# Kernel optimization log

Hardware: AMD Instinct MI355X
Metric: run time of the kernel (lower is better)

Reference implementation:

```python
import jax, jax.numpy as jnp
import numpy as np

B, S, E, H = 2, 2048, 1024, 16
D = E // H  # d_k = n_wires = 64


def setup_inputs() -> dict:
    key = jax.random.key(0)
    ks = jax.random.split(key, 6)
    x = jax.random.normal(ks[0], (B, S, E), dtype=jnp.float32)
    scale = 0.02
    Wq = jax.random.normal(ks[1], (E, E), dtype=jnp.float32) * scale
    Wk = jax.random.normal(ks[2], (E, E), dtype=jnp.float32) * scale
    Wv = jax.random.normal(ks[3], (E, E), dtype=jnp.float32) * scale
    Wc = jax.random.normal(ks[4], (E, E), dtype=jnp.float32) * scale
    bc = jnp.zeros((E,), dtype=jnp.float32)
    return {"x": x, "Wq": Wq, "Wk": Wk, "Wv": Wv, "Wc": Wc, "bc": bc}


def _split_heads(t):
    # [B,S,E] -> [B,H,S,D]
    return t.reshape(B, S, H, D).transpose(0, 2, 1, 3)


def _quantum(t):
    # RX(theta_i) per wire + CNOT ladder + per-wire PauliZ expectation:
    # <Z_j> = prod_{i<=j} cos(theta_i)  (closed form of the circuit)
    return jnp.cumprod(jnp.cos(t), axis=-1)


def reference(x, Wq, Wk, Wv, Wc, bc):
    q = _quantum(_split_heads(x @ Wq.T))  # [B,H,S,D]
    k = _quantum(_split_heads(x @ Wk.T))
    v = _quantum(_split_heads(x @ Wv.T))
    scores = jnp.einsum('bhsd,bhtd->bhst', q, k) / jnp.sqrt(jnp.float32(D))
    attn = jax.nn.softmax(scores, axis=-1)
    out = jnp.einsum('bhst,bhtd->bhsd', attn, v)  # [B,H,S,D]
    out = out.transpose(0, 2, 1, 3).reshape(B, S, E)
    return out @ Wc.T + bc
```

## Files before the change

kernel.cpp:

```cpp
#include <hip/hip_runtime.h>
#include <hip/hip_bf16.h>

constexpr int Bc = 2, Sc = 2048, Ec = 1024, Hc = 16, Dc = 64;
constexpr int Mrows = Bc * Sc;
constexpr int Kdim  = Ec;

typedef float  floatx4 __attribute__((ext_vector_type(4)));
typedef short  shortx8 __attribute__((ext_vector_type(8)));

__device__ inline unsigned short f2bf(float f) {
    union { __hip_bfloat16 h; unsigned short u; } cv;
    cv.h = __float2bfloat16(f);
    return cv.u;
}
__device__ inline float bf2f(unsigned short u) {
    union { unsigned int i; float f; } c; c.i = ((unsigned int)u) << 16; return c.f;
}
__device__ inline float exp2_fast(float x) {
#if __has_builtin(__builtin_amdgcn_exp2f)
    return __builtin_amdgcn_exp2f(x);
#else
    return __expf(x * 0.69314718056f);
#endif
}

__device__ __forceinline__ void gll16(const void* g, void* lds) {
    __builtin_amdgcn_global_load_lds(
        (const __attribute__((address_space(1))) void*)g,
        (__attribute__((address_space(3))) void*)lds, 16, 0, 0);
}

__global__ __launch_bounds__(256) void convert_all_kernel(
    const float* __restrict__ x,  const float* __restrict__ Wq,
    const float* __restrict__ Wk, const float* __restrict__ Wv,
    const float* __restrict__ Wc,
    unsigned short* __restrict__ xb,  unsigned short* __restrict__ Wqb,
    unsigned short* __restrict__ Wkb, unsigned short* __restrict__ Wvb,
    unsigned short* __restrict__ Wcb)
{
    const long t = (long)blockIdx.x * 256 + threadIdx.x;
    const long i = t * 4;
    const float* src; unsigned short* dst; long off;
    if (i < 4194304) { src = x; dst = xb; off = i; }
    else {
        long j = i - 4194304;
        int wsel = (int)(j >> 20);
        off = j & 1048575;
        src = (wsel == 0) ? Wq : (wsel == 1) ? Wk : (wsel == 2) ? Wv : Wc;
        dst = (wsel == 0) ? Wqb : (wsel == 1) ? Wkb : (wsel == 2) ? Wvb : Wcb;
    }
    float4 v = *(const float4*)(src + off);
    unsigned short tmp[4] __attribute__((aligned(8)));
    tmp[0] = f2bf(v.x); tmp[1] = f2bf(v.y); tmp[2] = f2bf(v.z); tmp[3] = f2bf(v.w);
    *(uint2*)(dst + off) = *(uint2*)tmp;
}

__global__ __launch_bounds__(256) void proj_mfma_kernel(
    const unsigned short* __restrict__ Ab,
    const unsigned short* __restrict__ Wqb,
    const unsigned short* __restrict__ Wkb,
    const unsigned short* __restrict__ Wvb,
    unsigned short* __restrict__ oq,
    unsigned short* __restrict__ ok,
    unsigned short* __restrict__ ov)
{
    __shared__ __align__(16) char smem[33792];
    float (*Cs)[132] = (float(*)[132])smem;
    __shared__ float Sp[64][9];

    const int z = blockIdx.z;
    const unsigned short* Wb = (z == 0) ? Wqb : (z == 1) ? Wkb : Wvb;
    unsigned short* out      = (z == 0) ? oq  : (z == 1) ? ok  : ov;
    const int mode = (z == 2) ? 1 : 0;

    const int tid = threadIdx.x;
    const int lane = tid & 63;
    const int w = tid >> 6, l15 = tid & 15, quad = (tid >> 4) & 3;
    const int wq = w >> 1, wn = w & 1;
    const int m0 = blockIdx.x * 128;
    const int n0 = blockIdx.y * 128;
    const int h0 = n0 >> 6;
    const int sw = l15 & 7;

    floatx4 acc[4][4];
    #pragma unroll
    for (int ms = 0; ms < 4; ++ms)
        #pragma unroll
        for (int ns = 0; ns < 4; ++ns)
            #pragma unroll
            for (int e = 0; e < 4; ++e) acc[ms][ns][e] = 0.0f;

    for (int k0 = 0; k0 < Kdim; k0 += 64) {
        #pragma unroll
        for (int j = 0; j < 4; ++j) {
            int idx = j * 64 + lane;
            int row = 32 * w + (idx >> 3);
            int cg  = ((idx & 7) ^ (idx >> 3)) & 7;
            gll16(Ab + (size_t)(m0 + row) * Kdim + k0 + cg * 8,
                  smem + 4096 * w + 1024 * j);
            gll16(Wb + (size_t)(n0 + row) * Kdim + k0 + cg * 8,
                  smem + 16384 + 4096 * w + 1024 * j);
        }
        __syncthreads();
        #pragma unroll
        for (int ks = 0; ks < 2; ++ks) {
            shortx8 af[4], bf[4];
            #pragma unroll
            for (int ms = 0; ms < 4; ++ms)
                af[ms] = *(shortx8*)(smem + (64 * wq + 16 * ms + l15) * 128
                                     + (((4 * ks + quad) ^ sw) << 4));
            #pragma unroll
            for (int ns = 0; ns < 4; ++ns)
                bf[ns] = *(shortx8*)(smem + 16384 + (64 * wn + 16 * ns + l15) * 128
                                     + (((4 * ks + quad) ^ sw) << 4));
            #pragma unroll
            for (int ms = 0; ms < 4; ++ms)
                #pragma unroll
                for (int ns = 0; ns < 4; ++ns)
                    acc[ms][ns] = __builtin_amdgcn_mfma_f32_16x16x32_bf16(
                        af[ms], bf[ns], acc[ms][ns], 0, 0, 0);
        }
        __syncthreads();
    }

    const int b = m0 >> 11;
    const int sbase = m0 & (Sc - 1);

    for (int pass = 0; pass < 2; ++pass) {
        if (wq == pass) {
            #pragma unroll
            for (int ms = 0; ms < 4; ++ms)
                #pragma unroll
                for (int ns = 0; ns < 4; ++ns)
                    #pragma unroll
                    for (int r = 0; r < 4; ++r)
                        Cs[16 * ms + 4 * quad + r][64 * wn + 16 * ns + l15] =
                            __cosf(acc[ms][ns][r]);
        }
        __syncthreads();
        #pragma unroll
        for (int t = tid; t < 512; t += 256) {
            int row = t >> 3, seg = t & 7;
            float pr = 1.0f;
            #pragma unroll
            for (int c = 0; c < 16; ++c) pr *= Cs[row][seg * 16 + c];
            Sp[row][seg] = pr;
        }
        __syncthreads();
        if (mode == 0) {
            #pragma unroll
            for (int t = tid; t < 512; t += 256) {
                int row = t >> 3, seg = t & 7;
                float p = 1.0f;
                for (int j = (seg & 4); j < seg; ++j) p *= Sp[row][j];
                unsigned short tmp[16] __attribute__((aligned(16)));
                #pragma unroll
                for (int c = 0; c < 16; ++c) { p *= Cs[row][seg * 16 + c]; tmp[c] = f2bf(p); }
                int h = h0 + (seg >> 2);
                int s = sbase + pass * 64 + row;
                size_t base = (((size_t)b * Hc + h) * Sc + s) * Dc + (seg & 3) * 16;
                *(shortx8*)(out + base)     = *(shortx8*)&tmp[0];
                *(shortx8*)(out + base + 8) = *(shortx8*)&tmp[8];
            }
            __syncthreads();
        } else {
            #pragma unroll
            for (int t = tid; t < 512; t += 256) {
                int row = t >> 3, seg = t & 7;
                float p = 1.0f;
                for (int j = (seg & 4); j < seg; ++j) p *= Sp[row][j];
                #pragma unroll
                for (int c = 0; c < 16; ++c) { p *= Cs[row][seg * 16 + c]; Cs[row][seg * 16 + c] = p; }
            }
            __syncthreads();
            #pragma unroll
            for (int t = tid; t < 512; t += 256) {
                int col = t >> 2, chunk = t & 3;
                int h = h0 + (col >> 6), d = col & 63;
                unsigned short tmp[16] __attribute__((aligned(16)));
                #pragma unroll
                for (int j = 0; j < 16; ++j) tmp[j] = f2bf(Cs[chunk * 16 + j][col]);
                size_t base = (((size_t)b * Hc + h) * Dc + d) * Sc
                              + sbase + pass * 64 + chunk * 16;
                *(shortx8*)(out + base)     = *(shortx8*)&tmp[0];
                *(shortx8*)(out + base + 8) = *(shortx8*)&tmp[8];
            }
            __syncthreads();
        }
    }
}

__global__ __launch_bounds__(256) void attn_mfma_kernel(
    const unsigned short* __restrict__ qg,
    const unsigned short* __restrict__ kg,
    const unsigned short* __restrict__ vtg,
    unsigned short* __restrict__ o1,
    unsigned short* __restrict__ o2,
    float* __restrict__ lpart)
{
    __shared__ __align__(16) char smem[34816];
    unsigned short (*Pq)[72] = (unsigned short(*)[72])(smem + 16384);

    const int tid  = threadIdx.x;
    const int lane = tid & 63;
    const int w    = tid >> 6;
    const int l15  = tid & 15;
    const int quad = (tid >> 4) & 3;
    const int qb   = blockIdx.x;
    const int half = blockIdx.y;
    const int bh   = blockIdx.z;
    const int sw   = l15 & 7;

    const unsigned short* qp = qg  + (size_t)bh * Sc * Dc;
    const unsigned short* kp = kg  + (size_t)bh * Sc * Dc;
    const unsigned short* vp = vtg + (size_t)bh * Dc * Sc;

    int qrow[2];
    shortx8 qf[2][2];
    #pragma unroll
    for (int qs = 0; qs < 2; ++qs) {
        qrow[qs] = qb * 128 + 32 * w + 16 * qs + l15;
        qf[qs][0] = *(const shortx8*)(qp + (size_t)qrow[qs] * Dc + 8 * quad);
        qf[qs][1] = *(const shortx8*)(qp + (size_t)qrow[qs] * Dc + 32 + 8 * quad);
    }

    floatx4 Oacc[2][4];
    #pragma unroll
    for (int qs = 0; qs < 2; ++qs)
        #pragma unroll
        for (int mt = 0; mt < 4; ++mt)
            #pragma unroll
            for (int e = 0; e < 4; ++e) Oacc[qs][mt][e] = 0.0f;
    float lsum[2] = {0.0f, 0.0f};

    const float cexp = 0.125f * 1.442695041f;

    for (int kt = half * 16; kt < half * 16 + 16; ++kt) {
        #pragma unroll
        for (int j = 0; j < 2; ++j) {
            int idx = j * 64 + lane;
            int row = 16 * w + (idx >> 3);
            int cg  = ((idx & 7) ^ (idx >> 3)) & 7;
            gll16(kp + (size_t)(kt * 64 + row) * Dc + cg * 8,
                  smem + 2048 * w + 1024 * j);
            gll16(vp + (size_t)row * Sc + kt * 64 + cg * 8,
                  smem + 8192 + 2048 * w + 1024 * j);
        }
        __syncthreads();

        shortx8 kf[2][4], vf[2][4];
        #pragma unroll
        for (int ks = 0; ks < 2; ++ks)
            #pragma unroll
            for (int mt = 0; mt < 4; ++mt) {
                int off = (16 * mt + l15) * 128 + (((4 * ks + quad) ^ sw) << 4);
                kf[ks][mt] = *(shortx8*)(smem + off);
                vf[ks][mt] = *(shortx8*)(smem + 8192 + off);
            }

        #pragma unroll
        for (int qs = 0; qs < 2; ++qs) {
            floatx4 st[4];
            #pragma unroll
            for (int mt = 0; mt < 4; ++mt)
                #pragma unroll
                for (int e = 0; e < 4; ++e) st[mt][e] = 0.0f;
            #pragma unroll
            for (int ks = 0; ks < 2; ++ks)
                #pragma unroll
                for (int mt = 0; mt < 4; ++mt)
                    st[mt] = __builtin_amdgcn_mfma_f32_16x16x32_bf16(
                        kf[ks][mt], qf[qs][ks], st[mt], 0, 0, 0);

            float rs = 0.0f;
            #pragma unroll
            for (int mt = 0; mt < 4; ++mt) {
                float p0 = exp2_fast(st[mt][0] * cexp);
                float p1 = exp2_fast(st[mt][1] * cexp);
                float p2 = exp2_fast(st[mt][2] * cexp);
                float p3 = exp2_fast(st[mt][3] * cexp);
                rs += (p0 + p1) + (p2 + p3);
                unsigned short tmp[4] __attribute__((aligned(8)));
                tmp[0] = f2bf(p0); tmp[1] = f2bf(p1); tmp[2] = f2bf(p2); tmp[3] = f2bf(p3);
                *(uint2*)&Pq[32 * w + 16 * qs + l15][16 * mt + 4 * quad] = *(uint2*)tmp;
            }
            lsum[qs] += rs;

            #pragma unroll
            for (int ks = 0; ks < 2; ++ks) {
                shortx8 pf = *(shortx8*)&Pq[32 * w + 16 * qs + l15][32 * ks + 8 * quad];
                #pragma unroll
                for (int mt = 0; mt < 4; ++mt)
                    Oacc[qs][mt] = __builtin_amdgcn_mfma_f32_16x16x32_bf16(
                        vf[ks][mt], pf, Oacc[qs][mt], 0, 0, 0);
            }
        }
        __syncthreads();
    }

    const int b = bh >> 4, hh = bh & 15;
    unsigned short* opart = half ? o2 : o1;
    float* lp = lpart + ((size_t)half * (Bc * Hc) + bh) * Sc;
    #pragma unroll
    for (int qs = 0; qs < 2; ++qs) {
        float l = lsum[qs];
        l += __shfl_xor(l, 16, 64);
        l += __shfl_xor(l, 32, 64);
        if (quad == 0) lp[qrow[qs]] = l;
        #pragma unroll
        for (int mt = 0; mt < 4; ++mt) {
            unsigned short tmp[4] __attribute__((aligned(8)));
            #pragma unroll
            for (int r = 0; r < 4; ++r) tmp[r] = f2bf(Oacc[qs][mt][r]);
            size_t base = ((size_t)b * Sc + qrow[qs]) * Ec + hh * 64 + 16 * mt + 4 * quad;
            *(uint2*)(opart + base) = *(uint2*)tmp;
        }
    }
}

__global__ __launch_bounds__(256) void combine_kernel(
    unsigned short* __restrict__ o1,
    const unsigned short* __restrict__ o2,
    const float* __restrict__ lpart)
{
    const size_t t = (size_t)blockIdx.x * 256 + threadIdx.x;
    const size_t base = t * 8;
    const int e = (int)(base & (Ec - 1));
    const int h = e >> 6;
    const size_t bs = base >> 10;
    const int b = (int)(bs >> 11), s = (int)(bs & (Sc - 1));
    const int bh = b * Hc + h;
    const float l = lpart[(size_t)bh * Sc + s]
                  + lpart[(size_t)(Bc * Hc + bh) * Sc + s];
    const float inv = 1.0f / l;
    uint4 a = *(const uint4*)(o1 + base);
    uint4 c = *(const uint4*)(o2 + base);
    const unsigned short* ua = (const unsigned short*)&a;
    const unsigned short* uc = (const unsigned short*)&c;
    unsigned short r[8] __attribute__((aligned(16)));
    #pragma unroll
    for (int i = 0; i < 8; ++i)
        r[i] = f2bf((bf2f(ua[i]) + bf2f(uc[i])) * inv);
    *(uint4*)(o1 + base) = *(uint4*)r;
}

__global__ __launch_bounds__(256) void outproj_mfma_kernel(
    const unsigned short* __restrict__ Ab,
    const unsigned short* __restrict__ Wb,
    const float* __restrict__ bias,
    float* __restrict__ out)
{
    __shared__ __align__(16) char smem[24576];

    const int tid = threadIdx.x;
    const int lane = tid & 63;
    const int w = tid >> 6, l15 = tid & 15, quad = (tid >> 4) & 3;
    const int wq = w >> 1, wn = w & 1;
    const int m0 = blockIdx.x * 64;
    const int n0 = blockIdx.y * 128;
    const int sw = l15 & 7;

    floatx4 acc[2][4];
    #pragma unroll
    for (int ms = 0; ms < 2; ++ms)
        #pragma unroll
        for (int ns = 0; ns < 4; ++ns)
            #pragma unroll
            for (int e = 0; e < 4; ++e) acc[ms][ns][e] = 0.0f;

    for (int k0 = 0; k0 < Kdim; k0 += 64) {
        #pragma unroll
        for (int j = 0; j < 2; ++j) {
            int idx = j * 64 + lane;
            int row = 16 * w + (idx >> 3);
            int cg  = ((idx & 7) ^ (idx >> 3)) & 7;
            gll16(Ab + (size_t)(m0 + row) * Kdim + k0 + cg * 8,
                  smem + 2048 * w + 1024 * j);
        }
        #pragma unroll
        for (int j = 0; j < 4; ++j) {
            int idx = j * 64 + lane;
            int row = 32 * w + (idx >> 3);
            int cg  = ((idx & 7) ^ (idx >> 3)) & 7;
            gll16(Wb + (size_t)(n0 + row) * Kdim + k0 + cg * 8,
                  smem + 8192 + 4096 * w + 1024 * j);
        }
        __syncthreads();
        #pragma unroll
        for (int ks = 0; ks < 2; ++ks) {
            shortx8 af[2], bf[4];
            #pragma unroll
            for (int ms = 0; ms < 2; ++ms)
                af[ms] = *(shortx8*)(smem + (32 * wq + 16 * ms + l15) * 128
                                     + (((4 * ks + quad) ^ sw) << 4));
            #pragma unroll
            for (int ns = 0; ns < 4; ++ns)
                bf[ns] = *(shortx8*)(smem + 8192 + (64 * wn + 16 * ns + l15) * 128
                                     + (((4 * ks + quad) ^ sw) << 4));
            #pragma unroll
            for (int ms = 0; ms < 2; ++ms)
                #pragma unroll
                for (int ns = 0; ns < 4; ++ns)
                    acc[ms][ns] = __builtin_amdgcn_mfma_f32_16x16x32_bf16(
                        af[ms], bf[ns], acc[ms][ns], 0, 0, 0);
        }
        __syncthreads();
    }

    #pragma unroll
    for (int ns = 0; ns < 4; ++ns) {
        const float bv = bias[n0 + 64 * wn + 16 * ns + l15];
        #pragma unroll
        for (int ms = 0; ms < 2; ++ms)
            #pragma unroll
            for (int r = 0; r < 4; ++r) {
                int m = m0 + 32 * wq + 16 * ms + 4 * quad + r;
                out[(size_t)m * Kdim + n0 + 64 * wn + 16 * ns + l15] = acc[ms][ns][r] + bv;
            }
    }
}

extern "C" void kernel_launch(void* const* d_in, const int* in_sizes, int n_in,
                              void* d_out, int out_size, void* d_ws, size_t ws_size,
                              hipStream_t stream) {
    const float* x  = (const float*)d_in[0];
    const float* Wq = (const float*)d_in[1];
    const float* Wk = (const float*)d_in[2];
    const float* Wv = (const float*)d_in[3];
    const float* Wc = (const float*)d_in[4];
    const float* bc = (const float*)d_in[5];
    float* out = (float*)d_out;

    char* p = (char*)d_ws;
    unsigned short* xb   = (unsigned short*)(p);
    unsigned short* Wqb  = (unsigned short*)(p + (8u << 20));
    unsigned short* Wkb  = (unsigned short*)(p + (10u << 20));
    unsigned short* Wvb  = (unsigned short*)(p + (12u << 20));
    unsigned short* Wcb  = (unsigned short*)(p + (14u << 20));
    unsigned short* qb_  = (unsigned short*)(p + (16u << 20));
    unsigned short* kb_  = (unsigned short*)(p + (24u << 20));
    unsigned short* vtb  = (unsigned short*)(p + (32u << 20));
    unsigned short* attb = (unsigned short*)(p + (40u << 20));
    unsigned short* o2b  = xb;
    float*          lpart = (float*)(p + (8u << 20));

    hipLaunchKernelGGL(convert_all_kernel, dim3(8192), dim3(256), 0, stream,
                       x, Wq, Wk, Wv, Wc, xb, Wqb, Wkb, Wvb, Wcb);

    hipLaunchKernelGGL(proj_mfma_kernel, dim3(Mrows / 128, Ec / 128, 3), dim3(256), 0, stream,
                       xb, Wqb, Wkb, Wvb, qb_, kb_, vtb);

    hipLaunchKernelGGL(attn_mfma_kernel, dim3(Sc / 128, 2, Bc * Hc), dim3(256), 0, stream,
                       qb_, kb_, vtb, attb, o2b, lpart);

    hipLaunchKernelGGL(combine_kernel, dim3(Mrows * Ec / (256 * 8)), dim3(256), 0, stream,
                       attb, o2b, lpart);

    hipLaunchKernelGGL(outproj_mfma_kernel, dim3(Mrows / 64, Ec / 128), dim3(256), 0, stream,
                       attb, Wcb, bc, out);
}
```

Measured before the change: 212.8 us.

## Double-buffer K/V tiles, fold softmax scale into Q, use cheaper bf16 packing

The attention loop moves from 64-key tiles with two barriers per tile to 32-key tiles held in double-buffered LDS, so the next tile's global-to-LDS load is issued while the current one is computed. The softmax scale and log2(e) factor are folded into Q when the projection stores it, which removes one multiply per score. Every bf16 conversion is replaced by a hand-written round-half-up pack of two floats into one dword. In exchange the loop runs twice as many iterations with smaller MFMA batches, and the rounding differs slightly from round-to-nearest-even with no NaN handling. The new P-tile indexing (Pq[16*w+l15]) and per-wave loads should be checked against the 128-query block layout, because rows appear to be shared between the qs iterations.

```diff
diff --git a/kernel.cpp b/kernel.cpp
--- a/kernel.cpp
+++ b/kernel.cpp
@@ -5,13 +5,15 @@
 constexpr int Mrows = Bc * Sc;
 constexpr int Kdim  = Ec;
 
+#define QSCALE 0.18033688011112042f
+
 typedef float  floatx4 __attribute__((ext_vector_type(4)));
 typedef short  shortx8 __attribute__((ext_vector_type(8)));
 
-__device__ inline unsigned short f2bf(float f) {
-    union { __hip_bfloat16 h; unsigned short u; } cv;
-    cv.h = __float2bfloat16(f);
-    return cv.u;
+__device__ __forceinline__ unsigned int pack2bf(float a, float b) {
+    union { float f; unsigned int u; } ca, cb;
+    ca.f = a; cb.f = b;
+    return ((ca.u + 0x8000u) >> 16) | ((cb.u + 0x8000u) & 0xffff0000u);
 }
 __device__ inline float bf2f(unsigned short u) {
     union { unsigned int i; float f; } c; c.i = ((unsigned int)u) << 16; return c.f;
@@ -50,9 +52,10 @@
         dst = (wsel == 0) ? Wqb : (wsel == 1) ? Wkb : (wsel == 2) ? Wvb : Wcb;
     }
     float4 v = *(const float4*)(src + off);
-    unsigned short tmp[4] __attribute__((aligned(8)));
-    tmp[0] = f2bf(v.x); tmp[1] = f2bf(v.y); tmp[2] = f2bf(v.z); tmp[3] = f2bf(v.w);
-    *(uint2*)(dst + off) = *(uint2*)tmp;
+    uint2 u;
+    u.x = pack2bf(v.x, v.y);
+    u.y = pack2bf(v.z, v.w);
+    *(uint2*)(dst + off) = u;
 }
 
 __global__ __launch_bounds__(256) void proj_mfma_kernel(
@@ -72,6 +75,7 @@
     const unsigned short* Wb = (z == 0) ? Wqb : (z == 1) ? Wkb : Wvb;
     unsigned short* out      = (z == 0) ? oq  : (z == 1) ? ok  : ov;
     const int mode = (z == 2) ? 1 : 0;
+    const float osc = (z == 0) ? QSCALE : 1.0f;
 
     const int tid = threadIdx.x;
     const int lane = tid & 63;
@@ -153,14 +157,18 @@
                 int row = t >> 3, seg = t & 7;
                 float p = 1.0f;
                 for (int j = (seg & 4); j < seg; ++j) p *= Sp[row][j];
-                unsigned short tmp[16] __attribute__((aligned(16)));
-                #pragma unroll
-                for (int c = 0; c < 16; ++c) { p *= Cs[row][seg * 16 + c]; tmp[c] = f2bf(p); }
+                unsigned int dw[8];
+                #pragma unroll
+                for (int c2 = 0; c2 < 8; ++c2) {
+                    p *= Cs[row][seg * 16 + 2 * c2];     float a = p * osc;
+                    p *= Cs[row][seg * 16 + 2 * c2 + 1]; float bb = p * osc;
+                    dw[c2] = pack2bf(a, bb);
+                }
                 int h = h0 + (seg >> 2);
                 int s = sbase + pass * 64 + row;
                 size_t base = (((size_t)b * Hc + h) * Sc + s) * Dc + (seg & 3) * 16;
-                *(shortx8*)(out + base)     = *(shortx8*)&tmp[0];
-                *(shortx8*)(out + base + 8) = *(shortx8*)&tmp[8];
+                *(uint4*)(out + base)     = *(uint4*)&dw[0];
+                *(uint4*)(out + base + 8) = *(uint4*)&dw[4];
             }
             __syncthreads();
         } else {
@@ -177,13 +185,15 @@
             for (int t = tid; t < 512; t += 256) {
                 int col = t >> 2, chunk = t & 3;
                 int h = h0 + (col >> 6), d = col & 63;
-                unsigned short tmp[16] __attribute__((aligned(16)));
-                #pragma unroll
-                for (int j = 0; j < 16; ++j) tmp[j] = f2bf(Cs[chunk * 16 + j][col]);
+                unsigned int dw[8];
+                #pragma unroll
+                for (int j2 = 0; j2 < 8; ++j2)
+                    dw[j2] = pack2bf(Cs[chunk * 16 + 2 * j2][col],
+                                     Cs[chunk * 16 + 2 * j2 + 1][col]);
                 size_t base = (((size_t)b * Hc + h) * Dc + d) * Sc
                               + sbase + pass * 64 + chunk * 16;
-                *(shortx8*)(out + base)     = *(shortx8*)&tmp[0];
-                *(shortx8*)(out + base + 8) = *(shortx8*)&tmp[8];
+                *(uint4*)(out + base)     = *(uint4*)&dw[0];
+                *(uint4*)(out + base + 8) = *(uint4*)&dw[4];
             }
             __syncthreads();
         }
@@ -198,8 +208,9 @@
     unsigned short* __restrict__ o2,
     float* __restrict__ lpart)
 {
-    __shared__ __align__(16) char smem[34816];
-    unsigned short (*Pq)[72] = (unsigned short(*)[72])(smem + 16384);
+    __shared__ __align__(16) unsigned short Ks[2][32][64];
+    __shared__ __align__(16) unsigned short VTs[2][64][32];
+    __shared__ __align__(16) unsigned short Pq[64][72];
 
     const int tid  = threadIdx.x;
     const int lane = tid & 63;
@@ -233,69 +244,70 @@
             for (int e = 0; e < 4; ++e) Oacc[qs][mt][e] = 0.0f;
     float lsum[2] = {0.0f, 0.0f};
 
-    const float cexp = 0.125f * 1.442695041f;
-
-    for (int kt = half * 16; kt < half * 16 + 16; ++kt) {
-        #pragma unroll
-        for (int j = 0; j < 2; ++j) {
-            int idx = j * 64 + lane;
-            int row = 16 * w + (idx >> 3);
-            int cg  = ((idx & 7) ^ (idx >> 3)) & 7;
-            gll16(kp + (size_t)(kt * 64 + row) * Dc + cg * 8,
-                  smem + 2048 * w + 1024 * j);
-            gll16(vp + (size_t)row * Sc + kt * 64 + cg * 8,
-                  smem + 8192 + 2048 * w + 1024 * j);
-        }
-        __syncthreads();
-
-        shortx8 kf[2][4], vf[2][4];
+    const unsigned short* kgl = kp
+        + (size_t)(half * 1024 + 8 * w + (lane >> 3)) * Dc
+        + (((lane & 7) ^ ((lane >> 3) & 7)) * 8);
+    const unsigned short* vgl = vp
+        + (size_t)(16 * w + (lane >> 2)) * Sc + half * 1024 + (lane & 3) * 8;
+
+    gll16(kgl, &Ks[0][8 * w][0]);
+    gll16(vgl, &VTs[0][16 * w][0]);
+
+    for (int it = 0; it < 32; ++it) {
+        const int buf = it & 1;
+        __syncthreads();
+        if (it + 1 < 32) {
+            const int nb = (it + 1) & 1;
+            gll16(kgl + (size_t)(it + 1) * 32 * Dc, &Ks[nb][8 * w][0]);
+            gll16(vgl + (it + 1) * 32,              &VTs[nb][16 * w][0]);
+        }
+
+        shortx8 kf[2][2], vf[4];
         #pragma unroll
         for (int ks = 0; ks < 2; ++ks)
             #pragma unroll
-            for (int mt = 0; mt < 4; ++mt) {
-                int off = (16 * mt + l15) * 128 + (((4 * ks + quad) ^ sw) << 4);
-                kf[ks][mt] = *(shortx8*)(smem + off);
-                vf[ks][mt] = *(shortx8*)(smem + 8192 + off);
-            }
+            for (int mtp = 0; mtp < 2; ++mtp)
+                kf[ks][mtp] = *(shortx8*)&Ks[buf][16 * mtp + l15]
+                                            [(((4 * ks + quad) ^ sw) & 7) * 8];
+        #pragma unroll
+        for (int mt = 0; mt < 4; ++mt)
+            vf[mt] = *(shortx8*)&VTs[buf][16 * mt + l15][8 * quad];
 
         #pragma unroll
         for (int qs = 0; qs < 2; ++qs) {
-            floatx4 st[4];
-            #pragma unroll
-            for (int mt = 0; mt < 4; ++mt)
-                #pragma unroll
-                for (int e = 0; e < 4; ++e) st[mt][e] = 0.0f;
+            floatx4 st[2];
+            #pragma unroll
+            for (int mtp = 0; mtp < 2; ++mtp)
+                #pragma unroll
+                for (int e = 0; e < 4; ++e) st[mtp][e] = 0.0f;
             #pragma unroll
             for (int ks = 0; ks < 2; ++ks)
                 #pragma unroll
-                for (int mt = 0; mt < 4; ++mt)
-                    st[mt] = __builtin_amdgcn_mfma_f32_16x16x32_bf16(
-                        kf[ks][mt], qf[qs][ks], st[mt], 0, 0, 0);
+                for (int mtp = 0; mtp < 2; ++mtp)
+                    st[mtp] = __builtin_amdgcn_mfma_f32_16x16x32_bf16(
+                        kf[ks][mtp], qf[qs][ks], st[mtp], 0, 0, 0);
 
             float rs = 0.0f;
             #pragma unroll
-            for (int mt = 0; mt < 4; ++mt) {
-                float p0 = exp2_fast(st[mt][0] * cexp);
-                float p1 = exp2_fast(st[mt][1] * cexp);
-                float p2 = exp2_fast(st[mt][2] * cexp);
-                float p3 = exp2_fast(st[mt][3] * cexp);
+            for (int mtp = 0; mtp < 2; ++mtp) {
+                float p0 = exp2_fast(st[mtp][0]);
+                float p1 = exp2_fast(st[mtp][1]);
+                float p2 = exp2_fast(st[mtp][2]);
+                float p3 = exp2_fast(st[mtp][3]);
                 rs += (p0 + p1) + (p2 + p3);
-                unsigned short tmp[4] __attribute__((aligned(8)));
-                tmp[0] = f2bf(p0); tmp[1] = f2bf(p1); tmp[2] = f2bf(p2); tmp[3] = f2bf(p3);
-                *(uint2*)&Pq[32 * w + 16 * qs + l15][16 * mt + 4 * quad] = *(uint2*)tmp;
+                uint2 u;
+                u.x = pack2bf(p0, p1);
+                u.y = pack2bf(p2, p3);
+                *(uint2*)&Pq[16 * w + l15][16 * mtp + 4 * quad] = u;
             }
             lsum[qs] += rs;
 
-            #pragma unroll
-            for (int ks = 0; ks < 2; ++ks) {
-                shortx8 pf = *(shortx8*)&Pq[32 * w + 16 * qs + l15][32 * ks + 8 * quad];
-                #pragma unroll
-                for (int mt = 0; mt < 4; ++mt)
-                    Oacc[qs][mt] = __builtin_amdgcn_mfma_f32_16x16x32_bf16(
-                        vf[ks][mt], pf, Oacc[qs][mt], 0, 0, 0);
-            }
-        }
-        __syncthreads();
+            shortx8 pf = *(shortx8*)&Pq[16 * w + l15][8 * quad];
+            #pragma unroll
+            for (int mt = 0; mt < 4; ++mt)
+                Oacc[qs][mt] = __builtin_amdgcn_mfma_f32_16x16x32_bf16(
+                    vf[mt], pf, Oacc[qs][mt], 0, 0, 0);
+        }
     }
 
     const int b = bh >> 4, hh = bh & 15;
@@ -309,11 +321,11 @@
         if (quad == 0) lp[qrow[qs]] = l;
         #pragma unroll
         for (int mt = 0; mt < 4; ++mt) {
-            unsigned short tmp[4] __attribute__((aligned(8)));
-            #pragma unroll
-            for (int r = 0; r < 4; ++r) tmp[r] = f2bf(Oacc[qs][mt][r]);
+            uint2 u;
+            u.x = pack2bf(Oacc[qs][mt][0], Oacc[qs][mt][1]);
+            u.y = pack2bf(Oacc[qs][mt][2], Oacc[qs][mt][3]);
             size_t base = ((size_t)b * Sc + qrow[qs]) * Ec + hh * 64 + 16 * mt + 4 * quad;
-            *(uint2*)(opart + base) = *(uint2*)tmp;
+            *(uint2*)(opart + base) = u;
         }
     }
 }
@@ -337,11 +349,12 @@
     uint4 c = *(const uint4*)(o2 + base);
     const unsigned short* ua = (const unsigned short*)&a;
     const unsigned short* uc = (const unsigned short*)&c;
-    unsigned short r[8] __attribute__((aligned(16)));
-    #pragma unroll
-    for (int i = 0; i < 8; ++i)
-        r[i] = f2bf((bf2f(ua[i]) + bf2f(uc[i])) * inv);
-    *(uint4*)(o1 + base) = *(uint4*)r;
+    unsigned int dw[4];
+    #pragma unroll
+    for (int i = 0; i < 4; ++i)
+        dw[i] = pack2bf((bf2f(ua[2 * i]) + bf2f(uc[2 * i])) * inv,
+                        (bf2f(ua[2 * i + 1]) + bf2f(uc[2 * i + 1])) * inv);
+    *(uint4*)(o1 + base) = *(uint4*)dw;
 }
 
 __global__ __launch_bounds__(256) void outproj_mfma_kernel(
```

After: 214.2 us. About the same (+0.7%).

## Fuse pipeline into one cooperative persistent kernel with grid syncs

Applied to the files above, without the earlier changes.

Replaces the five separate launches with a single cooperative kernel of 512 blocks that runs convert, QKV projection, attention and output projection as phases separated by grid.sync. Attention no longer splits keys into two halves, so the combine kernel goes away. The softmax scale is folded into Q at projection time, bf16 packing uses a manual round-to-nearest, and the projection tile shrinks to 64x128. The aim is to remove launch gaps and the combine pass, at the cost of fewer blocks (512) and less parallelism in attention, plus grid-wide barriers.

```diff
diff --git a/kernel.cpp b/kernel.cpp
--- a/kernel.cpp
+++ b/kernel.cpp
@@ -1,20 +1,22 @@
 #include <hip/hip_runtime.h>
 #include <hip/hip_bf16.h>
+#include <hip/hip_cooperative_groups.h>
+
+namespace cg = cooperative_groups;
 
 constexpr int Bc = 2, Sc = 2048, Ec = 1024, Hc = 16, Dc = 64;
 constexpr int Mrows = Bc * Sc;
 constexpr int Kdim  = Ec;
 
+#define QSCALE 0.18033688011112042f
+
 typedef float  floatx4 __attribute__((ext_vector_type(4)));
 typedef short  shortx8 __attribute__((ext_vector_type(8)));
 
-__device__ inline unsigned short f2bf(float f) {
-    union { __hip_bfloat16 h; unsigned short u; } cv;
-    cv.h = __float2bfloat16(f);
-    return cv.u;
-}
-__device__ inline float bf2f(unsigned short u) {
-    union { unsigned int i; float f; } c; c.i = ((unsigned int)u) << 16; return c.f;
+__device__ __forceinline__ unsigned int pack2bf(float a, float b) {
+    union { float f; unsigned int u; } ca, cb;
+    ca.f = a; cb.f = b;
+    return ((ca.u + 0x8000u) >> 16) | ((cb.u + 0x8000u) & 0xffff0000u);
 }
 __device__ inline float exp2_fast(float x) {
 #if __has_builtin(__builtin_amdgcn_exp2f)
@@ -30,7 +32,9 @@
         (__attribute__((address_space(3))) void*)lds, 16, 0, 0);
 }
 
-__global__ __launch_bounds__(256) void convert_all_kernel(
+
+__device__ __forceinline__ void phase_convert(
+    int bx, int tid,
     const float* __restrict__ x,  const float* __restrict__ Wq,
     const float* __restrict__ Wk, const float* __restrict__ Wv,
     const float* __restrict__ Wc,
@@ -38,135 +42,145 @@
     unsigned short* __restrict__ Wkb, unsigned short* __restrict__ Wvb,
     unsigned short* __restrict__ Wcb)
 {
-    const long t = (long)blockIdx.x * 256 + threadIdx.x;
-    const long i = t * 4;
-    const float* src; unsigned short* dst; long off;
-    if (i < 4194304) { src = x; dst = xb; off = i; }
-    else {
-        long j = i - 4194304;
-        int wsel = (int)(j >> 20);
-        off = j & 1048575;
-        src = (wsel == 0) ? Wq : (wsel == 1) ? Wk : (wsel == 2) ? Wv : Wc;
-        dst = (wsel == 0) ? Wqb : (wsel == 1) ? Wkb : (wsel == 2) ? Wvb : Wcb;
-    }
-    float4 v = *(const float4*)(src + off);
-    unsigned short tmp[4] __attribute__((aligned(8)));
-    tmp[0] = f2bf(v.x); tmp[1] = f2bf(v.y); tmp[2] = f2bf(v.z); tmp[3] = f2bf(v.w);
-    *(uint2*)(dst + off) = *(uint2*)tmp;
-}
-
-__global__ __launch_bounds__(256) void proj_mfma_kernel(
-    const unsigned short* __restrict__ Ab,
+    const long gtid = (long)bx * 256 + tid;
+    for (long t = gtid; t < 2097152; t += 131072) {
+        const long i = t * 4;
+        const float* src; unsigned short* dst; long off;
+        if (i < 4194304) { src = x; dst = xb; off = i; }
+        else {
+            long j = i - 4194304;
+            int wsel = (int)(j >> 20);
+            off = j & 1048575;
+            src = (wsel == 0) ? Wq : (wsel == 1) ? Wk : (wsel == 2) ? Wv : Wc;
+            dst = (wsel == 0) ? Wqb : (wsel == 1) ? Wkb : (wsel == 2) ? Wvb : Wcb;
+        }
+        float4 v = *(const float4*)(src + off);
+        uint2 u;
+        u.x = pack2bf(v.x, v.y);
+        u.y = pack2bf(v.z, v.w);
+        *(uint2*)(dst + off) = u;
+    }
+}
+
+__device__ __forceinline__ void phase_proj(
+    char* smem, int bx, int tid,
+    const unsigned short* __restrict__ xb,
     const unsigned short* __restrict__ Wqb,
     const unsigned short* __restrict__ Wkb,
     const unsigned short* __restrict__ Wvb,
-    unsigned short* __restrict__ oq,
-    unsigned short* __restrict__ ok,
-    unsigned short* __restrict__ ov)
-{
-    __shared__ __align__(16) char smem[33792];
-    float (*Cs)[132] = (float(*)[132])smem;
-    __shared__ float Sp[64][9];
-
-    const int z = blockIdx.z;
-    const unsigned short* Wb = (z == 0) ? Wqb : (z == 1) ? Wkb : Wvb;
-    unsigned short* out      = (z == 0) ? oq  : (z == 1) ? ok  : ov;
-    const int mode = (z == 2) ? 1 : 0;
-
-    const int tid = threadIdx.x;
+    unsigned short* __restrict__ qg, unsigned short* __restrict__ kg,
+    unsigned short* __restrict__ vtg)
+{
     const int lane = tid & 63;
     const int w = tid >> 6, l15 = tid & 15, quad = (tid >> 4) & 3;
     const int wq = w >> 1, wn = w & 1;
-    const int m0 = blockIdx.x * 128;
-    const int n0 = blockIdx.y * 128;
-    const int h0 = n0 >> 6;
     const int sw = l15 & 7;
-
-    floatx4 acc[4][4];
-    #pragma unroll
-    for (int ms = 0; ms < 4; ++ms)
-        #pragma unroll
-        for (int ns = 0; ns < 4; ++ns)
-            #pragma unroll
-            for (int e = 0; e < 4; ++e) acc[ms][ns][e] = 0.0f;
-
-    for (int k0 = 0; k0 < Kdim; k0 += 64) {
-        #pragma unroll
-        for (int j = 0; j < 4; ++j) {
-            int idx = j * 64 + lane;
-            int row = 32 * w + (idx >> 3);
-            int cg  = ((idx & 7) ^ (idx >> 3)) & 7;
-            gll16(Ab + (size_t)(m0 + row) * Kdim + k0 + cg * 8,
-                  smem + 4096 * w + 1024 * j);
-            gll16(Wb + (size_t)(n0 + row) * Kdim + k0 + cg * 8,
-                  smem + 16384 + 4096 * w + 1024 * j);
-        }
-        __syncthreads();
-        #pragma unroll
-        for (int ks = 0; ks < 2; ++ks) {
-            shortx8 af[4], bf[4];
-            #pragma unroll
-            for (int ms = 0; ms < 4; ++ms)
-                af[ms] = *(shortx8*)(smem + (64 * wq + 16 * ms + l15) * 128
-                                     + (((4 * ks + quad) ^ sw) << 4));
+    float (*Cs)[132] = (float(*)[132])smem;
+    float (*Sp)[9]   = (float(*)[9])(smem + 33792);
+
+    for (int t = bx; t < 1536; t += 512) {
+        const int z   = t >> 9;
+        const int rem = t & 511;
+        const int m0  = (rem & 63) * 64;
+        const int n0  = (rem >> 6) * 128;
+        const unsigned short* Wb = (z == 0) ? Wqb : (z == 1) ? Wkb : Wvb;
+        unsigned short* po       = (z == 0) ? qg  : (z == 1) ? kg  : vtg;
+        const float osc = (z == 0) ? QSCALE : 1.0f;
+
+        floatx4 acc[2][4];
+        #pragma unroll
+        for (int ms = 0; ms < 2; ++ms)
             #pragma unroll
             for (int ns = 0; ns < 4; ++ns)
-                bf[ns] = *(shortx8*)(smem + 16384 + (64 * wn + 16 * ns + l15) * 128
-                                     + (((4 * ks + quad) ^ sw) << 4));
-            #pragma unroll
-            for (int ms = 0; ms < 4; ++ms)
+                #pragma unroll
+                for (int e = 0; e < 4; ++e) acc[ms][ns][e] = 0.0f;
+
+        for (int k0 = 0; k0 < Kdim; k0 += 64) {
+            #pragma unroll
+            for (int j = 0; j < 2; ++j) {
+                int idx = j * 64 + lane;
+                int row = 16 * w + (idx >> 3);
+                int cg2 = ((idx & 7) ^ (idx >> 3)) & 7;
+                gll16(xb + (size_t)(m0 + row) * Kdim + k0 + cg2 * 8,
+                      smem + 2048 * w + 1024 * j);
+            }
+            #pragma unroll
+            for (int j = 0; j < 4; ++j) {
+                int idx = j * 64 + lane;
+                int row = 32 * w + (idx >> 3);
+                int cg2 = ((idx & 7) ^ (idx >> 3)) & 7;
+                gll16(Wb + (size_t)(n0 + row) * Kdim + k0 + cg2 * 8,
+                      smem + 8192 + 4096 * w + 1024 * j);
+            }
+            __syncthreads();
+            #pragma unroll
+            for (int ks = 0; ks < 2; ++ks) {
+                shortx8 af[2], bf[4];
+                #pragma unroll
+                for (int ms = 0; ms < 2; ++ms)
+                    af[ms] = *(shortx8*)(smem + (32 * wq + 16 * ms + l15) * 128
+                                         + (((4 * ks + quad) ^ sw) << 4));
                 #pragma unroll
                 for (int ns = 0; ns < 4; ++ns)
-                    acc[ms][ns] = __builtin_amdgcn_mfma_f32_16x16x32_bf16(
-                        af[ms], bf[ns], acc[ms][ns], 0, 0, 0);
-        }
-        __syncthreads();
-    }
-
-    const int b = m0 >> 11;
-    const int sbase = m0 & (Sc - 1);
-
-    for (int pass = 0; pass < 2; ++pass) {
-        if (wq == pass) {
-            #pragma unroll
-            for (int ms = 0; ms < 4; ++ms)
-                #pragma unroll
-                for (int ns = 0; ns < 4; ++ns)
+                    bf[ns] = *(shortx8*)(smem + 8192 + (64 * wn + 16 * ns + l15) * 128
+                                         + (((4 * ks + quad) ^ sw) << 4));
+                #pragma unroll
+                for (int ms = 0; ms < 2; ++ms)
                     #pragma unroll
-                    for (int r = 0; r < 4; ++r)
-                        Cs[16 * ms + 4 * quad + r][64 * wn + 16 * ns + l15] =
-                            __cosf(acc[ms][ns][r]);
-        }
-        __syncthreads();
-        #pragma unroll
-        for (int t = tid; t < 512; t += 256) {
-            int row = t >> 3, seg = t & 7;
+                    for (int ns = 0; ns < 4; ++ns)
+                        acc[ms][ns] = __builtin_amdgcn_mfma_f32_16x16x32_bf16(
+                            af[ms], bf[ns], acc[ms][ns], 0, 0, 0);
+            }
+            __syncthreads();
+        }
+
+        #pragma unroll
+        for (int ms = 0; ms < 2; ++ms)
+            #pragma unroll
+            for (int ns = 0; ns < 4; ++ns)
+                #pragma unroll
+                for (int r = 0; r < 4; ++r)
+                    Cs[32 * wq + 16 * ms + 4 * quad + r][64 * wn + 16 * ns + l15] =
+                        __cosf(acc[ms][ns][r]);
+        __syncthreads();
+        #pragma unroll
+        for (int t2 = tid; t2 < 512; t2 += 256) {
+            int row = t2 >> 3, seg = t2 & 7;
             float pr = 1.0f;
             #pragma unroll
             for (int c = 0; c < 16; ++c) pr *= Cs[row][seg * 16 + c];
             Sp[row][seg] = pr;
         }
         __syncthreads();
-        if (mode == 0) {
-            #pragma unroll
-            for (int t = tid; t < 512; t += 256) {
-                int row = t >> 3, seg = t & 7;
+
+        const int b = m0 >> 11;
+        const int sbase = m0 & (Sc - 1);
+        const int h0 = n0 >> 6;
+
+        if (z != 2) {
+            #pragma unroll
+            for (int t2 = tid; t2 < 512; t2 += 256) {
+                int row = t2 >> 3, seg = t2 & 7;
                 float p = 1.0f;
                 for (int j = (seg & 4); j < seg; ++j) p *= Sp[row][j];
-                unsigned short tmp[16] __attribute__((aligned(16)));
-                #pragma unroll
-                for (int c = 0; c < 16; ++c) { p *= Cs[row][seg * 16 + c]; tmp[c] = f2bf(p); }
+                unsigned int dw[8];
+                #pragma unroll
+                for (int c2 = 0; c2 < 8; ++c2) {
+                    p *= Cs[row][seg * 16 + 2 * c2];     float a = p * osc;
+                    p *= Cs[row][seg * 16 + 2 * c2 + 1]; float bb = p * osc;
+                    dw[c2] = pack2bf(a, bb);
+                }
                 int h = h0 + (seg >> 2);
-                int s = sbase + pass * 64 + row;
+                int s = sbase + row;
                 size_t base = (((size_t)b * Hc + h) * Sc + s) * Dc + (seg & 3) * 16;
-                *(shortx8*)(out + base)     = *(shortx8*)&tmp[0];
-                *(shortx8*)(out + base + 8) = *(shortx8*)&tmp[8];
+                *(uint4*)(po + base)     = *(uint4*)&dw[0];
+                *(uint4*)(po + base + 8) = *(uint4*)&dw[4];
             }
             __syncthreads();
         } else {
             #pragma unroll
-            for (int t = tid; t < 512; t += 256) {
-                int row = t >> 3, seg = t & 7;
+            for (int t2 = tid; t2 < 512; t2 += 256) {
+                int row = t2 >> 3, seg = t2 & 7;
                 float p = 1.0f;
                 for (int j = (seg & 4); j < seg; ++j) p *= Sp[row][j];
                 #pragma unroll
@@ -174,46 +188,40 @@
             }
             __syncthreads();
             #pragma unroll
-            for (int t = tid; t < 512; t += 256) {
-                int col = t >> 2, chunk = t & 3;
+            for (int t2 = tid; t2 < 512; t2 += 256) {
+                int col = t2 >> 2, chunk = t2 & 3;
                 int h = h0 + (col >> 6), d = col & 63;
-                unsigned short tmp[16] __attribute__((aligned(16)));
-                #pragma unroll
-                for (int j = 0; j < 16; ++j) tmp[j] = f2bf(Cs[chunk * 16 + j][col]);
+                unsigned int dw[8];
+                #pragma unroll
+                for (int j2 = 0; j2 < 8; ++j2)
+                    dw[j2] = pack2bf(Cs[chunk * 16 + 2 * j2][col],
+                                     Cs[chunk * 16 + 2 * j2 + 1][col]);
                 size_t base = (((size_t)b * Hc + h) * Dc + d) * Sc
-                              + sbase + pass * 64 + chunk * 16;
-                *(shortx8*)(out + base)     = *(shortx8*)&tmp[0];
-                *(shortx8*)(out + base + 8) = *(shortx8*)&tmp[8];
+                              + sbase + chunk * 16;
+                *(uint4*)(po + base)     = *(uint4*)&dw[0];
+                *(uint4*)(po + base + 8) = *(uint4*)&dw[4];
             }
             __syncthreads();
         }
     }
 }
 
-__global__ __launch_bounds__(256) void attn_mfma_kernel(
-    const unsigned short* __restrict__ qg,
-    const unsigned short* __restrict__ kg,
-    const unsigned short* __restrict__ vtg,
-    unsigned short* __restrict__ o1,
-    unsigned short* __restrict__ o2,
-    float* __restrict__ lpart)
-{
-    __shared__ __align__(16) char smem[34816];
-    unsigned short (*Pq)[72] = (unsigned short(*)[72])(smem + 16384);
-
-    const int tid  = threadIdx.x;
+__device__ __forceinline__ void phase_attn(
+    char* smem, int bx, int tid,
+    const unsigned short* __restrict__ qg, const unsigned short* __restrict__ kg,
+    const unsigned short* __restrict__ vtg, unsigned short* __restrict__ attb)
+{
     const int lane = tid & 63;
-    const int w    = tid >> 6;
-    const int l15  = tid & 15;
-    const int quad = (tid >> 4) & 3;
-    const int qb   = blockIdx.x;
-    const int half = blockIdx.y;
-    const int bh   = blockIdx.z;
-    const int sw   = l15 & 7;
+    const int w = tid >> 6, l15 = tid & 15, quad = (tid >> 4) & 3;
+    const int sw = l15 & 7;
+    const int qb = bx & 15;
+    const int bh = bx >> 4;
 
     const unsigned short* qp = qg  + (size_t)bh * Sc * Dc;
     const unsigned short* kp = kg  + (size_t)bh * Sc * Dc;
     const unsigned short* vp = vtg + (size_t)bh * Dc * Sc;
+
+    unsigned short (*Pq)[72] = (unsigned short(*)[72])(smem + 16384);
 
     int qrow[2];
     shortx8 qf[2][2];
@@ -233,17 +241,15 @@
             for (int e = 0; e < 4; ++e) Oacc[qs][mt][e] = 0.0f;
     float lsum[2] = {0.0f, 0.0f};
 
-    const float cexp = 0.125f * 1.442695041f;
-
-    for (int kt = half * 16; kt < half * 16 + 16; ++kt) {
+    for (int kt = 0; kt < 32; ++kt) {
         #pragma unroll
         for (int j = 0; j < 2; ++j) {
             int idx = j * 64 + lane;
             int row = 16 * w + (idx >> 3);
-            int cg  = ((idx & 7) ^ (idx >> 3)) & 7;
-            gll16(kp + (size_t)(kt * 64 + row) * Dc + cg * 8,
+            int cg2 = ((idx & 7) ^ (idx >> 3)) & 7;
+            gll16(kp + (size_t)(kt * 64 + row) * Dc + cg2 * 8,
                   smem + 2048 * w + 1024 * j);
-            gll16(vp + (size_t)row * Sc + kt * 64 + cg * 8,
+            gll16(vp + (size_t)row * Sc + kt * 64 + cg2 * 8,
                   smem + 8192 + 2048 * w + 1024 * j);
         }
         __syncthreads();
@@ -275,14 +281,15 @@
             float rs = 0.0f;
             #pragma unroll
             for (int mt = 0; mt < 4; ++mt) {
-                float p0 = exp2_fast(st[mt][0] * cexp);
-                float p1 = exp2_fast(st[mt][1] * cexp);
-                float p2 = exp2_fast(st[mt][2] * cexp);
-                float p3 = exp2_fast(st[mt][3] * cexp);
+                float p0 = exp2_fast(st[mt][0]);
+                float p1 = exp2_fast(st[mt][1]);
+                float p2 = exp2_fast(st[mt][2]);
+                float p3 = exp2_fast(st[mt][3]);
                 rs += (p0 + p1) + (p2 + p3);
-                unsigned short tmp[4] __attribute__((aligned(8)));
-                tmp[0] = f2bf(p0); tmp[1] = f2bf(p1); tmp[2] = f2bf(p2); tmp[3] = f2bf(p3);
-                *(uint2*)&Pq[32 * w + 16 * qs + l15][16 * mt + 4 * quad] = *(uint2*)tmp;
+                uint2 u;
+                u.x = pack2bf(p0, p1);
+                u.y = pack2bf(p2, p3);
+                *(uint2*)&Pq[32 * w + 16 * qs + l15][16 * mt + 4 * quad] = u;
             }
             lsum[qs] += rs;
 
@@ -299,66 +306,35 @@
     }
 
     const int b = bh >> 4, hh = bh & 15;
-    unsigned short* opart = half ? o2 : o1;
-    float* lp = lpart + ((size_t)half * (Bc * Hc) + bh) * Sc;
     #pragma unroll
     for (int qs = 0; qs < 2; ++qs) {
         float l = lsum[qs];
         l += __shfl_xor(l, 16, 64);
         l += __shfl_xor(l, 32, 64);
-        if (quad == 0) lp[qrow[qs]] = l;
+        const float inv = 1.0f / l;
         #pragma unroll
         for (int mt = 0; mt < 4; ++mt) {
-            unsigned short tmp[4] __attribute__((aligned(8)));
-            #pragma unroll
-            for (int r = 0; r < 4; ++r) tmp[r] = f2bf(Oacc[qs][mt][r]);
+            uint2 u;
+            u.x = pack2bf(Oacc[qs][mt][0] * inv, Oacc[qs][mt][1] * inv);
+            u.y = pack2bf(Oacc[qs][mt][2] * inv, Oacc[qs][mt][3] * inv);
             size_t base = ((size_t)b * Sc + qrow[qs]) * Ec + hh * 64 + 16 * mt + 4 * quad;
-            *(uint2*)(opart + base) = *(uint2*)tmp;
-        }
-    }
-}
-
-__global__ __launch_bounds__(256) void combine_kernel(
-    unsigned short* __restrict__ o1,
-    const unsigned short* __restrict__ o2,
-    const float* __restrict__ lpart)
-{
-    const size_t t = (size_t)blockIdx.x * 256 + threadIdx.x;
-    const size_t base = t * 8;
-    const int e = (int)(base & (Ec - 1));
-    const int h = e >> 6;
-    const size_t bs = base >> 10;
-    const int b = (int)(bs >> 11), s = (int)(bs & (Sc - 1));
-    const int bh = b * Hc + h;
-    const float l = lpart[(size_t)bh * Sc + s]
-                  + lpart[(size_t)(Bc * Hc + bh) * Sc + s];
-    const float inv = 1.0f / l;
-    uint4 a = *(const uint4*)(o1 + base);
-    uint4 c = *(const uint4*)(o2 + base);
-    const unsigned short* ua = (const unsigned short*)&a;
-    const unsigned short* uc = (const unsigned short*)&c;
-    unsigned short r[8] __attribute__((aligned(16)));
-    #pragma unroll
-    for (int i = 0; i < 8; ++i)
-        r[i] = f2bf((bf2f(ua[i]) + bf2f(uc[i])) * inv);
-    *(uint4*)(o1 + base) = *(uint4*)r;
-}
-
-__global__ __launch_bounds__(256) void outproj_mfma_kernel(
-    const unsigned short* __restrict__ Ab,
-    const unsigned short* __restrict__ Wb,
-    const float* __restrict__ bias,
-    float* __restrict__ out)
-{
-    __shared__ __align__(16) char smem[24576];
-
-    const int tid = threadIdx.x;
+            *(uint2*)(attb + base) = u;
+        }
+    }
+}
+
+__device__ __forceinline__ void phase_outproj(
+    char* smem, int bx, int tid,
+    const unsigned short* __restrict__ attb,
+    const unsigned short* __restrict__ Wcb,
+    const float* __restrict__ bias, float* __restrict__ out)
+{
     const int lane = tid & 63;
     const int w = tid >> 6, l15 = tid & 15, quad = (tid >> 4) & 3;
     const int wq = w >> 1, wn = w & 1;
-    const int m0 = blockIdx.x * 64;
-    const int n0 = blockIdx.y * 128;
     const int sw = l15 & 7;
+    const int m0 = (bx & 63) * 64;
+    const int n0 = (bx >> 6) * 128;
 
     floatx4 acc[2][4];
     #pragma unroll
@@ -373,16 +349,16 @@
         for (int j = 0; j < 2; ++j) {
             int idx = j * 64 + lane;
             int row = 16 * w + (idx >> 3);
-            int cg  = ((idx & 7) ^ (idx >> 3)) & 7;
-            gll16(Ab + (size_t)(m0 + row) * Kdim + k0 + cg * 8,
+            int cg2 = ((idx & 7) ^ (idx >> 3)) & 7;
+            gll16(attb + (size_t)(m0 + row) * Kdim + k0 + cg2 * 8,
                   smem + 2048 * w + 1024 * j);
         }
         #pragma unroll
         for (int j = 0; j < 4; ++j) {
             int idx = j * 64 + lane;
             int row = 32 * w + (idx >> 3);
-            int cg  = ((idx & 7) ^ (idx >> 3)) & 7;
-            gll16(Wb + (size_t)(n0 + row) * Kdim + k0 + cg * 8,
+            int cg2 = ((idx & 7) ^ (idx >> 3)) & 7;
+            gll16(Wcb + (size_t)(n0 + row) * Kdim + k0 + cg2 * 8,
                   smem + 8192 + 4096 * w + 1024 * j);
         }
         __syncthreads();
@@ -415,9 +391,67 @@
             #pragma unroll
             for (int r = 0; r < 4; ++r) {
                 int m = m0 + 32 * wq + 16 * ms + 4 * quad + r;
-                out[(size_t)m * Kdim + n0 + 64 * wn + 16 * ns + l15] = acc[ms][ns][r] + bv;
-            }
-    }
+                out[(size_t)m * Kdim + n0 + 64 * wn + 16 * ns + l15] =
+                    acc[ms][ns][r] + bv;
+            }
+    }
+}
+
+__global__ __launch_bounds__(256, 2) void fused_kernel(
+    const float* __restrict__ x,  const float* __restrict__ Wq,
+    const float* __restrict__ Wk, const float* __restrict__ Wv,
+    const float* __restrict__ Wc, const float* __restrict__ bc,
+    unsigned short* __restrict__ xb,  unsigned short* __restrict__ Wqb,
+    unsigned short* __restrict__ Wkb, unsigned short* __restrict__ Wvb,
+    unsigned short* __restrict__ Wcb,
+    unsigned short* __restrict__ qg, unsigned short* __restrict__ kg,
+    unsigned short* __restrict__ vtg, unsigned short* __restrict__ attb,
+    float* __restrict__ out)
+{
+    cg::grid_group grid = cg::this_grid();
+    __shared__ __align__(16) char smem[36096];
+    const int bx = blockIdx.x, tid = threadIdx.x;
+
+    phase_convert(bx, tid, x, Wq, Wk, Wv, Wc, xb, Wqb, Wkb, Wvb, Wcb);
+    __threadfence();
+    grid.sync();
+    phase_proj(smem, bx, tid, xb, Wqb, Wkb, Wvb, qg, kg, vtg);
+    __threadfence();
+    grid.sync();
+    phase_attn(smem, bx, tid, qg, kg, vtg, attb);
+    __threadfence();
+    grid.sync();
+    phase_outproj(smem, bx, tid, attb, Wcb, bc, out);
+}
+
+__global__ __launch_bounds__(256) void k_convert(
+    const float* x, const float* Wq, const float* Wk, const float* Wv,
+    const float* Wc, unsigned short* xb, unsigned short* Wqb,
+    unsigned short* Wkb, unsigned short* Wvb, unsigned short* Wcb)
+{
+    phase_convert(blockIdx.x, threadIdx.x, x, Wq, Wk, Wv, Wc, xb, Wqb, Wkb, Wvb, Wcb);
+}
+__global__ __launch_bounds__(256) void k_proj(
+    const unsigned short* xb, const unsigned short* Wqb,
+    const unsigned short* Wkb, const unsigned short* Wvb,
+    unsigned short* qg, unsigned short* kg, unsigned short* vtg)
+{
+    __shared__ __align__(16) char smem[36096];
+    phase_proj(smem, blockIdx.x, threadIdx.x, xb, Wqb, Wkb, Wvb, qg, kg, vtg);
+}
+__global__ __launch_bounds__(256) void k_attn(
+    const unsigned short* qg, const unsigned short* kg,
+    const unsigned short* vtg, unsigned short* attb)
+{
+    __shared__ __align__(16) char smem[36096];
+    phase_attn(smem, blockIdx.x, threadIdx.x, qg, kg, vtg, attb);
+}
+__global__ __launch_bounds__(256) void k_outproj(
+    const unsigned short* attb, const unsigned short* Wcb,
+    const float* bias, float* out)
+{
+    __shared__ __align__(16) char smem[36096];
+    phase_outproj(smem, blockIdx.x, threadIdx.x, attb, Wcb, bias, out);
 }
 
 extern "C" void kernel_launch(void* const* d_in, const int* in_sizes, int n_in,
@@ -441,21 +475,23 @@
     unsigned short* kb_  = (unsigned short*)(p + (24u << 20));
     unsigned short* vtb  = (unsigned short*)(p + (32u << 20));
     unsigned short* attb = (unsigned short*)(p + (40u << 20));
-    unsigned short* o2b  = xb;
-    float*          lpart = (float*)(p + (8u << 20));
-
-    hipLaunchKernelGGL(convert_all_kernel, dim3(8192), dim3(256), 0, stream,
-                       x, Wq, Wk, Wv, Wc, xb, Wqb, Wkb, Wvb, Wcb);
-
-    hipLaunchKernelGGL(proj_mfma_kernel, dim3(Mrows / 128, Ec / 128, 3), dim3(256), 0, stream,
-                       xb, Wqb, Wkb, Wvb, qb_, kb_, vtb);
-
-    hipLaunchKernelGGL(attn_mfma_kernel, dim3(Sc / 128, 2, Bc * Hc), dim3(256), 0, stream,
-                       qb_, kb_, vtb, attb, o2b, lpart);
-
-    hipLaunchKernelGGL(combine_kernel, dim3(Mrows * Ec / (256 * 8)), dim3(256), 0, stream,
-                       attb, o2b, lpart);
-
-    hipLaunchKernelGGL(outproj_mfma_kernel, dim3(Mrows / 64, Ec / 128), dim3(256), 0, stream,
-                       attb, Wcb, bc, out);
-}
+
+    void* args[] = {
+        (void*)&x, (void*)&Wq, (void*)&Wk, (void*)&Wv, (void*)&Wc, (void*)&bc,
+        (void*)&xb, (void*)&Wqb, (void*)&Wkb, (void*)&Wvb, (void*)&Wcb,
+        (void*)&qb_, (void*)&kb_, (void*)&vtb, (void*)&attb, (void*)&out
+    };
+    hipError_t err = hipLaunchCooperativeKernel((const void*)fused_kernel,
+                                                dim3(512), dim3(256),
+                                                args, 0, stream);
+    if (err != hipSuccess) {
+        hipLaunchKernelGGL(k_convert, dim3(512), dim3(256), 0, stream,
+                           x, Wq, Wk, Wv, Wc, xb, Wqb, Wkb, Wvb, Wcb);
+        hipLaunchKernelGGL(k_proj, dim3(512), dim3(256), 0, stream,
+                           xb, Wqb, Wkb, Wvb, qb_, kb_, vtb);
+        hipLaunchKernelGGL(k_attn, dim3(512), dim3(256), 0, stream,
+                           qb_, kb_, vtb, attb);
+        hipLaunchKernelGGL(k_outproj, dim3(512), dim3(256), 0, stream,
+                           attb, Wcb, bc, out);
+    }
+}
```

Measured after the change: 523.0 us. 146% more time.
